# Optimization experiments

Measured on AMD Instinct MI355X. Metric: run time of the kernel, lower is better.

## Reference

```python
import jax, jax.numpy as jnp
import numpy as np

TOPK = 50
TEMP = 5.0

def _l2norm(x):
    return x / jnp.linalg.norm(x, axis=-1, keepdims=True)

def setup_inputs() -> dict:
    key = jax.random.key(0)
    k1, k2, k3 = jax.random.split(key, 3)
    b, m, d = 32, 196, 512
    n, c = 51, 1000
    return {
        "image_features": jax.random.normal(k1, (b, d), dtype=jnp.float32),
        "local_image_features": jax.random.normal(k2, (b, m, d), dtype=jnp.float32),
        "all_text_features": jax.random.normal(k3, (n, c, d), dtype=jnp.float32),
        "logit_scale": jnp.full((1,), 4.6052, dtype=jnp.float32),  # ln(100), CLIP default
    }

def reference(image_features, local_image_features, all_text_features, logit_scale):
    # Inference path of CustomCLIP.forward (labels=None) -> get_dense_logits2
    img = _l2norm(image_features)                 # [b, d]
    loc = _l2norm(local_image_features)           # [b, m, d]
    txt = _l2norm(all_text_features)              # [n, c, d]  (n = ndisc = 51)
    mean_txt = _l2norm(txt.mean(axis=0))          # [c, d]

    base_logits = img @ mean_txt.T                # [b, c]
    w_raw = jnp.einsum('bd,bmd->bm', img, loc)    # [b, m]
    txt_cnd = jnp.transpose(txt, (1, 0, 2))       # [c, n, d]
    v = jax.nn.softmax(jnp.einsum('cd,cnd->cn', mean_txt, txt_cnd) * TEMP, axis=1)  # [c, n]

    # similarity of every patch to every description, laid out with m last for top_k
    sim = jnp.einsum('bmd,cnd->bcnm', loc, txt_cnd)        # [b, c, n, m]
    sim_topk, idx_topk = jax.lax.top_k(sim, TOPK)          # [b, c, n, k] each

    b = img.shape[0]
    # gather per-image patch weights at selected patch indices: w_raw[b, idx]
    w_topk = w_raw[jnp.arange(b)[:, None, None, None], idx_topk]   # [b, c, n, k]
    w = jax.nn.softmax(w_topk * TEMP, axis=3)               # softmax over selected patches

    bias_logits = jnp.sum(sim_topk * w * v[None, :, :, None], axis=(2, 3))  # [b, c]
    return jnp.exp(logit_scale)[0] * (base_logits + bias_logits)
```

## Files before the change

kernel.cpp:

```cpp
#include <hip/hip_runtime.h>
#include <stdint.h>

typedef __bf16  bf16x8 __attribute__((ext_vector_type(8)));
typedef float   f32x4  __attribute__((ext_vector_type(4)));
typedef short   s16x2  __attribute__((ext_vector_type(2)));
typedef unsigned short u16;

#define TEMP 5.0f

__device__ inline float wsum(float v){
  #pragma unroll
  for (int off=32; off; off>>=1) v += __shfl_xor(v, off, 64);
  return v;
}
__device__ inline float wmax(float v){
  #pragma unroll
  for (int off=32; off; off>>=1) v = fmaxf(v, __shfl_xor(v, off, 64));
  return v;
}
__device__ inline u16 f2bf(float f){
  unsigned u = __float_as_uint(f);
  u = u + 0x7fffu + ((u>>16)&1u);
  return (u16)(u>>16);
}
__device__ inline float bfl(unsigned u){ return __uint_as_float(u<<16); }
__device__ inline float bfh(unsigned u){ return __uint_as_float(u & 0xffff0000u); }

__device__ inline s16x2 as_s16x2(int v){ union{int i; s16x2 v;} u; u.i=v; return u.v; }

#if __has_builtin(__builtin_amdgcn_permlane16_swap) && __has_builtin(__builtin_amdgcn_permlane32_swap)
__device__ inline int qsum_i(int c){
  auto a = __builtin_amdgcn_permlane16_swap((unsigned)c, (unsigned)c, false, false);
  c = (int)a[0] + (int)a[1];
  auto b = __builtin_amdgcn_permlane32_swap((unsigned)c, (unsigned)c, false, false);
  return (int)b[0] + (int)b[1];
}
__device__ inline float qsum_f(float v){
  auto a = __builtin_amdgcn_permlane16_swap(__float_as_uint(v), __float_as_uint(v), false, false);
  v = __uint_as_float(a[0]) + __uint_as_float(a[1]);
  auto b = __builtin_amdgcn_permlane32_swap(__float_as_uint(v), __float_as_uint(v), false, false);
  return __uint_as_float(b[0]) + __uint_as_float(b[1]);
}
__device__ inline int qmin_i(int v){
  auto a = __builtin_amdgcn_permlane16_swap((unsigned)v, (unsigned)v, false, false);
  v = min((int)a[0], (int)a[1]);
  auto b = __builtin_amdgcn_permlane32_swap((unsigned)v, (unsigned)v, false, false);
  return min((int)b[0], (int)b[1]);
}
__device__ inline int qmax_i(int v){
  auto a = __builtin_amdgcn_permlane16_swap((unsigned)v, (unsigned)v, false, false);
  v = max((int)a[0], (int)a[1]);
  auto b = __builtin_amdgcn_permlane32_swap((unsigned)v, (unsigned)v, false, false);
  return max((int)b[0], (int)b[1]);
}
#else
__device__ inline int qsum_i(int c){
  c += __shfl_xor(c, 16, 64); c += __shfl_xor(c, 32, 64); return c;
}
__device__ inline float qsum_f(float v){
  v += __shfl_xor(v, 16, 64); v += __shfl_xor(v, 32, 64); return v;
}
__device__ inline int qmin_i(int v){
  v = min(v, __shfl_xor(v, 16, 64)); v = min(v, __shfl_xor(v, 32, 64)); return v;
}
__device__ inline int qmax_i(int v){
  v = max(v, __shfl_xor(v, 16, 64)); v = max(v, __shfl_xor(v, 32, 64)); return v;
}
#endif

__device__ inline s16x2 pkmin2(s16x2 a, s16x2 b){
  s16x2 r; r.x = a.x < b.x ? a.x : b.x; r.y = a.y < b.y ? a.y : b.y; return r;
}
__device__ inline s16x2 pkmax2(s16x2 a, s16x2 b){
  s16x2 r; r.x = a.x > b.x ? a.x : b.x; r.y = a.y > b.y ? a.y : b.y; return r;
}

__device__ inline void cp16(void* lds_uniform, const void* g){
  __builtin_amdgcn_global_load_lds(
    (const __attribute__((address_space(1))) unsigned int*)g,
    (__attribute__((address_space(3))) unsigned int*)lds_uniform, 16, 0, 0);
}

__global__ void k_img(const float* __restrict__ X, float* __restrict__ imgn){
  int b = blockIdx.x, lane = threadIdx.x;
  const float* src = X + (size_t)b*512 + lane*8;
  float4 a = *(const float4*)src;
  float4 c = *(const float4*)(src+4);
  float ss = a.x*a.x+a.y*a.y+a.z*a.z+a.w*a.w + c.x*c.x+c.y*c.y+c.z*c.z+c.w*c.w;
  ss = wsum(ss);
  float inv = 1.0f/sqrtf(ss);
  float* dst = imgn + (size_t)b*512 + lane*8;
  float4 o0 = {a.x*inv,a.y*inv,a.z*inv,a.w*inv};
  float4 o1 = {c.x*inv,c.y*inv,c.z*inv,c.w*inv};
  *(float4*)dst = o0; *(float4*)(dst+4) = o1;
}

__global__ void k_txt(const float* __restrict__ X, u16* __restrict__ TXT, float* __restrict__ invn){
  int cn = blockIdx.x, lane = threadIdx.x;
  int kc = lane>>2, kk8 = (lane&3)*8;
  size_t dstE = ((size_t)kc*51008 + cn)*32 + kk8;
  if (cn >= 51000){
    uint4 z = {0,0,0,0};
    *(uint4*)(TXT + dstE) = z;
    return;
  }
  int c = cn/51, n = cn - c*51;
  const float* src = X + ((size_t)n*1000 + c)*512 + lane*8;
  float4 a = *(const float4*)src;
  float4 d = *(const float4*)(src+4);
  float ss = a.x*a.x+a.y*a.y+a.z*a.z+a.w*a.w + d.x*d.x+d.y*d.y+d.z*d.z+d.w*d.w;
  ss = wsum(ss);
  float inv = 1.0f/sqrtf(ss);
  u16 h0=f2bf(a.x*inv),h1=f2bf(a.y*inv),h2=f2bf(a.z*inv),h3=f2bf(a.w*inv);
  u16 h4=f2bf(d.x*inv),h5=f2bf(d.y*inv),h6=f2bf(d.z*inv),h7=f2bf(d.w*inv);
  uint4 o;
  o.x = (unsigned)h0 | ((unsigned)h1<<16);
  o.y = (unsigned)h2 | ((unsigned)h3<<16);
  o.z = (unsigned)h4 | ((unsigned)h5<<16);
  o.w = (unsigned)h6 | ((unsigned)h7<<16);
  *(uint4*)(TXT + dstE) = o;
  if (lane==0) invn[(size_t)n*1000 + c] = inv;
}

__global__ void k_mean(const float* __restrict__ X, const float* __restrict__ invn, float* __restrict__ MT){
  int c = blockIdx.x, tid = threadIdx.x, lane = tid&63, wv = tid>>6;
  __shared__ float sinv[51];
  __shared__ float red[4];
  if (tid < 51) sinv[tid] = invn[(size_t)tid*1000 + c];
  __syncthreads();
  int d0 = tid*2;
  float sx=0.f, sy=0.f;
  for (int n=0;n<51;++n){
    const float2 x = *(const float2*)(X + ((size_t)n*1000 + c)*512 + d0);
    float iv = sinv[n];
    sx += x.x*iv; sy += x.y*iv;
  }
  float ss = sx*sx + sy*sy;
  ss = wsum(ss);
  if (lane==0) red[wv] = ss;
  __syncthreads();
  float tot = red[0]+red[1]+red[2]+red[3];
  float inv = 1.0f/sqrtf(tot);
  float2 o = {sx*inv, sy*inv};
  *(float2*)(MT + (size_t)c*512 + d0) = o;
}

__global__ void k_v(const u16* __restrict__ TXT, const float* __restrict__ MT, float* __restrict__ vbuf){
  int c = blockIdx.x, lane = threadIdx.x;
  __shared__ float lg[51];
  const float* mp = MT + (size_t)c*512 + lane*8;
  float4 m0 = *(const float4*)mp;
  float4 m1 = *(const float4*)(mp+4);
  int kc = lane>>2, kk8 = (lane&3)*8;
  for (int n=0;n<51;++n){
    size_t e = ((size_t)kc*51008 + (size_t)(c*51+n))*32 + kk8;
    uint4 q = *(const uint4*)(TXT + e);
    float d = bfl(q.x)*m0.x + bfh(q.x)*m0.y + bfl(q.y)*m0.z + bfh(q.y)*m0.w
            + bfl(q.z)*m1.x + bfh(q.z)*m1.y + bfl(q.w)*m1.z + bfh(q.w)*m1.w;
    d = wsum(d);
    if (lane==0) lg[n] = d;
  }
  __syncthreads();
  float val = (lane<51) ? lg[lane] : -1e30f;
  float mx = wmax(val);
  float e = (lane<51) ? expf(TEMP*(val-mx)) : 0.f;
  float s = wsum(e);
  if (lane<51) vbuf[(size_t)c*51 + lane] = e/s;
}

__global__ void k_base(const float* __restrict__ imgn, const float* __restrict__ MT, float* __restrict__ bias){
  int c = blockIdx.x, lane = threadIdx.x;
  const float* mp = MT + (size_t)c*512 + lane*8;
  float4 m0 = *(const float4*)mp;
  float4 m1 = *(const float4*)(mp+4);
  for (int b=0;b<32;++b){
    const float* ip = imgn + (size_t)b*512 + lane*8;
    float4 i0 = *(const float4*)ip;
    float4 i1 = *(const float4*)(ip+4);
    float d = i0.x*m0.x+i0.y*m0.y+i0.z*m0.z+i0.w*m0.w
            + i1.x*m1.x+i1.y*m1.y+i1.z*m1.z+i1.w*m1.w;
    d = wsum(d);
    if (lane==0) bias[(size_t)b*1000 + c] = d;
  }
}

__global__ void k_loc(const float* __restrict__ L, const float* __restrict__ imgn,
                      u16* __restrict__ LOC, float* __restrict__ ewg){
  int m = blockIdx.x, b = blockIdx.y, lane = threadIdx.x;
  size_t dstE = ((size_t)(b*16 + (lane>>2))*224 + m)*32 + (lane&3)*8;
  if (m >= 196){
    uint4 z = {0,0,0,0};
    *(uint4*)(LOC + dstE) = z;
    if (lane==0) ewg[(size_t)b*224 + m] = 0.f;
    return;
  }
  const float* src = L + ((size_t)b*196 + m)*512 + lane*8;
  float4 a = *(const float4*)src;
  float4 d = *(const float4*)(src+4);
  const float* ip = imgn + (size_t)b*512 + lane*8;
  float4 i0 = *(const float4*)ip;
  float4 i1 = *(const float4*)(ip+4);
  float ss = a.x*a.x+a.y*a.y+a.z*a.z+a.w*a.w + d.x*d.x+d.y*d.y+d.z*d.z+d.w*d.w;
  float ws = a.x*i0.x+a.y*i0.y+a.z*i0.z+a.w*i0.w + d.x*i1.x+d.y*i1.y+d.z*i1.z+d.w*i1.w;
  ss = wsum(ss); ws = wsum(ws);
  float inv = 1.0f/sqrtf(ss);
  u16 h0=f2bf(a.x*inv),h1=f2bf(a.y*inv),h2=f2bf(a.z*inv),h3=f2bf(a.w*inv);
  u16 h4=f2bf(d.x*inv),h5=f2bf(d.y*inv),h6=f2bf(d.z*inv),h7=f2bf(d.w*inv);
  uint4 o;
  o.x = (unsigned)h0 | ((unsigned)h1<<16);
  o.y = (unsigned)h2 | ((unsigned)h3<<16);
  o.z = (unsigned)h4 | ((unsigned)h5<<16);
  o.w = (unsigned)h6 | ((unsigned)h7<<16);
  *(uint4*)(LOC + dstE) = o;
  if (lane==0) ewg[(size_t)b*224 + m] = expf(TEMP * ws * inv);
}

__global__ __launch_bounds__(512,8) void k_main(const u16* __restrict__ TXT, const u16* __restrict__ LOC,
                                                const float* __restrict__ ewg, const float* __restrict__ vbuf,
                                                float* __restrict__ bias){
  __shared__ __align__(16) char smem[30592];
  const int tid = threadIdx.x, lane = tid & 63, wv = tid >> 6;
  const int quad = lane >> 4, l16 = lane & 15;
  const int ms = wv >> 2, ns = wv & 3;
  const int lsw = lane ^ ((lane>>3)&3);
  const int qsw = (quad ^ ((l16>>1)&3)) * 16;

  int id = blockIdx.x, b, cnt_;
  if (id < 24576){
    int g = id >> 10, r = id & 1023;
    b = r >> 5;  cnt_ = (g << 5) + (r & 31);
  } else {
    int r = id - 24576;
    b = r / 29;  cnt_ = 768 + r % 29;
  }
  const int cn0 = cnt_ * 64;

  float* ewl = (float*)(smem + 29696);
  if (tid < 224) ewl[tid] = ewg[(size_t)b*224 + tid];

  const f32x4 zero = {0.f,0.f,0.f,0.f};
  f32x4 acc[7];
  #pragma unroll
  for (int t=0;t<7;++t) acc[t]=zero;

  const u16* Abase = LOC + (size_t)(b*16)*224*32;
  char* Albd0 = smem;
  char* Albd1 = smem + 14336;

  auto stageA = [&](int kc, char* dst){
    const char* src = (const char*)(Abase + (size_t)kc*224*32);
    #pragma unroll
    for (int j=0;j<2;++j){
      int ch0 = j*512 + wv*64;
      if (ch0 < 896)
        cp16(dst + (size_t)ch0*16, src + (size_t)(ch0 + lsw)*16);
    }
  };
  auto loadB = [&](int kc)->bf16x8{
    size_t e = ((size_t)kc*51008 + (size_t)(cn0 + 16*ns + l16))*32 + quad*8;
    return *(const bf16x8*)(TXT + e);
  };
  auto domfma = [&](const char* Ab, bf16x8 bb){
    #pragma unroll
    for (int t=0;t<7;++t){
      bf16x8 af = *(const bf16x8*)(Ab + (size_t)((112*ms + 16*t + l16)*64) + qsw);
      acc[t] = __builtin_amdgcn_mfma_f32_16x16x32_bf16(af, bb, acc[t], 0,0,0);
    }
  };

  stageA(0, Albd0);
  bf16x8 bcur = loadB(0);
  __syncthreads();

  for (int kc = 0; kc < 16; ++kc){
    char* cur = (kc & 1) ? Albd1 : Albd0;
    char* nxt = (kc & 1) ? Albd0 : Albd1;
    bf16x8 bnext;
    if (kc < 15){
      stageA(kc+1, nxt);
      bnext = loadB(kc+1);
    }
    domfma(cur, bcur);
    bcur = bnext;
    __syncthreads();
  }

  const float KSC = 15360.0f;
  int kown[7][2], koth[7][2];
  {
    unsigned* wr = (unsigned*)(void*)smem + (size_t)(((ns<<1)|(ms^1))*16*58) + l16*58 + quad*2;
    #pragma unroll
    for (int t=0;t<7;++t){
      int a0 = (int)(acc[t][0]*KSC), a1 = (int)(acc[t][1]*KSC);
      int a2 = (int)(acc[t][2]*KSC), a3 = (int)(acc[t][3]*KSC);
      uint2 o; o.x = (unsigned)((a0 & 0xffff) | (a1<<16)); o.y = (unsigned)((a2 & 0xffff) | (a3<<16));
      *(uint2*)(wr + t*8) = o;
      kown[t][0] = (int)o.x; kown[t][1] = (int)o.y;
    }
  }
  __syncthreads();
  {
    const unsigned* rd = (const unsigned*)(void*)smem + (size_t)(((ns<<1)|ms)*16*58) + l16*58 + quad*2;
    #pragma unroll
    for (int t=0;t<7;++t){
      uint2 q = *(const uint2*)(rd + t*8);
      koth[t][0] = (int)q.x;
      koth[t][1] = (int)q.y;
    }
  }

  const int PKPK = (int)0xC180C180;
  if (ms == 1){
    if (quad != 0){ kown[5][0] = PKPK; kown[5][1] = PKPK; }
    kown[6][0] = PKPK; kown[6][1] = PKPK;
  } else {
    if (quad != 0){ koth[5][0] = PKPK; koth[5][1] = PKPK; }
    koth[6][0] = PKPK; koth[6][1] = PKPK;
  }

  s16x2 vmn = as_s16x2(kown[0][0]), vmx = vmn;
  #pragma unroll
  for (int t=0;t<5;++t){
    #pragma unroll
    for (int i=0;i<2;++i){
      vmn = pkmin2(vmn, as_s16x2(kown[t][i]));  vmx = pkmax2(vmx, as_s16x2(kown[t][i]));
      vmn = pkmin2(vmn, as_s16x2(koth[t][i]));  vmx = pkmax2(vmx, as_s16x2(koth[t][i]));
    }
  }
  int kmn = min((int)vmn.x, (int)vmn.y);
  int kmx = max((int)vmx.x, (int)vmx.y);
  kmn = qmin_i(kmn); kmx = qmax_i(kmx);
  int lo = kmn - 1, hi = kmx + 1;

  float flo = 146.0f, fhi = -50.0f;
  int side = 0;
  bool done = false;

  #pragma unroll 1
  for (int it = 0; it < 14; ++it){
    float fr = flo * __builtin_amdgcn_rcpf(flo - fhi);
    fr = fminf(fmaxf(fr, 0.04f), 0.96f);
    int tm = lo + (int)(fr * (float)(hi - lo));
    tm = (tm <= lo) ? (lo + 1) : ((tm >= hi) ? (hi - 1) : tm);

    s16x2 tmv = as_s16x2((tm & 0xffff) | (tm << 16));
    s16x2 ca = {0,0};
    #pragma unroll
    for (int t=0;t<7;++t){
      ca = ca + ((as_s16x2(kown[t][0]) - tmv) >> 15);
      ca = ca + ((as_s16x2(kown[t][1]) - tmv) >> 15);
      ca = ca + ((as_s16x2(koth[t][0]) - tmv) >> 15);
      ca = ca + ((as_s16x2(koth[t][1]) - tmv) >> 15);
    }
    int clt = -((int)ca.x + (int)ca.y);
    int c = qsum_i(56 - clt);

    bool ge = (c >= 50);
    if (!done){
      if (ge){ fhi = (side==1)  ? fhi*0.5f : fhi; flo = (float)(c-50); lo = tm; side = 1; }
      else   { flo = (side==-1) ? flo*0.5f : flo; fhi = (float)(c-50); hi = tm; side = -1; }
    }
    done = done || (c == 50) || ((hi - lo) <= 1);
    if (__all(done)) break;
  }
  const int thr = lo;

  float num = 0.f, den = 0.f;
  #pragma unroll
  for (int t=0;t<7;++t){
    f32x4 eA = *(const f32x4*)(ewl + 112*ms     + 16*t + 4*quad);
    f32x4 eB = *(const f32x4*)(ewl + 112*(ms^1) + 16*t + 4*quad);
    int a0 = (kown[t][0]<<16)>>16, a1 = kown[t][0]>>16;
    int a2 = (kown[t][1]<<16)>>16, a3 = kown[t][1]>>16;
    int b0 = (koth[t][0]<<16)>>16, b1 = koth[t][0]>>16;
    int b2 = (koth[t][1]<<16)>>16, b3 = koth[t][1]>>16;
    if (a0 >= thr){ num = fmaf((float)a0, eA[0], num); den += eA[0]; }
    if (a1 >= thr){ num = fmaf((float)a1, eA[1], num); den += eA[1]; }
    if (a2 >= thr){ num = fmaf((float)a2, eA[2], num); den += eA[2]; }
    if (a3 >= thr){ num = fmaf((float)a3, eA[3], num); den += eA[3]; }
    if (b0 >= thr){ num = fmaf((float)b0, eB[0], num); den += eB[0]; }
    if (b1 >= thr){ num = fmaf((float)b1, eB[1], num); den += eB[1]; }
    if (b2 >= thr){ num = fmaf((float)b2, eB[2], num); den += eB[2]; }
    if (b3 >= thr){ num = fmaf((float)b3, eB[3], num); den += eB[3]; }
  }
  num = qsum_f(num);
  den = qsum_f(den);

  int cn = cn0 + 16*ns + l16;
  if (quad == 0 && ms == 0 && cn < 51000){
    int c = cn/51;
    atomicAdd(bias + (size_t)b*1000 + c, vbuf[cn]*(num/(den*KSC)));
  }
}

__global__ void k_out(const float* __restrict__ bias, const float* __restrict__ ls, float* __restrict__ out){
  int i = blockIdx.x*256 + threadIdx.x;
  if (i < 32000){
    float sc = expf(ls[0]);
    out[i] = sc * bias[i];
  }
}

extern "C" void kernel_launch(void* const* d_in, const int* in_sizes, int n_in,
                              void* d_out, int out_size, void* d_ws, size_t ws_size,
                              hipStream_t stream) {
  const float* img = (const float*)d_in[0];
  const float* loc = (const float*)d_in[1];
  const float* txt = (const float*)d_in[2];
  const float* ls  = (const float*)d_in[3];
  char* ws = (char*)d_ws;
  float* imgn = (float*)(ws + 0);
  float* MT   = (float*)(ws + 65536);
  float* invn = (float*)(ws + 2113536);
  float* vbuf = (float*)(ws + 2317568);
  float* ewg  = (float*)(ws + 2521600);
  float* bias = (float*)(ws + 2550272);
  u16*   TXT  = (u16*)  (ws + 2678272);
  u16*   LOC  = (u16*)  (ws + 54910464);

  k_img <<<dim3(32),      dim3(64),  0, stream>>>(img, imgn);
  k_txt <<<dim3(51008),   dim3(64),  0, stream>>>(txt, TXT, invn);
  k_mean<<<dim3(1000),    dim3(256), 0, stream>>>(txt, invn, MT);
  k_v   <<<dim3(1000),    dim3(64),  0, stream>>>(TXT, MT, vbuf);
  k_base<<<dim3(1000),    dim3(64),  0, stream>>>(imgn, MT, bias);
  k_loc <<<dim3(224,32),  dim3(64),  0, stream>>>(loc, imgn, LOC, ewg);
  k_main<<<dim3(25504),   dim3(512), 0, stream>>>(TXT, LOC, ewg, vbuf, bias);
  k_out <<<dim3(125),     dim3(256), 0, stream>>>(bias, ls, (float*)d_out);
}
```

Before: 1.063 ms.

## Split per-column top-k threshold search across 8 lanes instead of 4

Changes how the per-column top-k threshold search is spread across lanes. Each column's 224 quantized similarities were held by 4 lanes (56 values each, own plus other half). They are now spread over 8 lanes (28 values each) through a new shared-memory layout. Reductions use DPP xor-1/xor-2 moves plus one permlane16 swap in place of the two-stage permlane16/32 swap. This halves the per-lane register footprint and the packed compare work in each bisection iteration, at the cost of an extra reduction stage and a different LDS read pattern.

```diff
diff --git a/kernel.cpp b/kernel.cpp
--- a/kernel.cpp
+++ b/kernel.cpp
@@ -28,51 +28,52 @@
 
 __device__ inline s16x2 as_s16x2(int v){ union{int i; s16x2 v;} u; u.i=v; return u.v; }
 
-#if __has_builtin(__builtin_amdgcn_permlane16_swap) && __has_builtin(__builtin_amdgcn_permlane32_swap)
-__device__ inline int qsum_i(int c){
-  auto a = __builtin_amdgcn_permlane16_swap((unsigned)c, (unsigned)c, false, false);
-  c = (int)a[0] + (int)a[1];
-  auto b = __builtin_amdgcn_permlane32_swap((unsigned)c, (unsigned)c, false, false);
-  return (int)b[0] + (int)b[1];
-}
-__device__ inline float qsum_f(float v){
-  auto a = __builtin_amdgcn_permlane16_swap(__float_as_uint(v), __float_as_uint(v), false, false);
-  v = __uint_as_float(a[0]) + __uint_as_float(a[1]);
-  auto b = __builtin_amdgcn_permlane32_swap(__float_as_uint(v), __float_as_uint(v), false, false);
-  return __uint_as_float(b[0]) + __uint_as_float(b[1]);
-}
-__device__ inline int qmin_i(int v){
-  auto a = __builtin_amdgcn_permlane16_swap((unsigned)v, (unsigned)v, false, false);
-  v = min((int)a[0], (int)a[1]);
-  auto b = __builtin_amdgcn_permlane32_swap((unsigned)v, (unsigned)v, false, false);
-  return min((int)b[0], (int)b[1]);
-}
-__device__ inline int qmax_i(int v){
-  auto a = __builtin_amdgcn_permlane16_swap((unsigned)v, (unsigned)v, false, false);
-  v = max((int)a[0], (int)a[1]);
-  auto b = __builtin_amdgcn_permlane32_swap((unsigned)v, (unsigned)v, false, false);
-  return max((int)b[0], (int)b[1]);
-}
-#else
-__device__ inline int qsum_i(int c){
-  c += __shfl_xor(c, 16, 64); c += __shfl_xor(c, 32, 64); return c;
-}
-__device__ inline float qsum_f(float v){
-  v += __shfl_xor(v, 16, 64); v += __shfl_xor(v, 32, 64); return v;
-}
-__device__ inline int qmin_i(int v){
-  v = min(v, __shfl_xor(v, 16, 64)); v = min(v, __shfl_xor(v, 32, 64)); return v;
-}
-__device__ inline int qmax_i(int v){
-  v = max(v, __shfl_xor(v, 16, 64)); v = max(v, __shfl_xor(v, 32, 64)); return v;
-}
-#endif
-
 __device__ inline s16x2 pkmin2(s16x2 a, s16x2 b){
   s16x2 r; r.x = a.x < b.x ? a.x : b.x; r.y = a.y < b.y ? a.y : b.y; return r;
 }
 __device__ inline s16x2 pkmax2(s16x2 a, s16x2 b){
   s16x2 r; r.x = a.x > b.x ? a.x : b.x; r.y = a.y > b.y ? a.y : b.y; return r;
+}
+
+#if __has_builtin(__builtin_amdgcn_mov_dpp)
+__device__ inline int dxor1(int v){ return __builtin_amdgcn_mov_dpp(v, 0xB1, 0xF, 0xF, true); }
+__device__ inline int dxor2(int v){ return __builtin_amdgcn_mov_dpp(v, 0x4E, 0xF, 0xF, true); }
+#else
+__device__ inline int dxor1(int v){ return __shfl_xor(v, 1, 64); }
+__device__ inline int dxor2(int v){ return __shfl_xor(v, 2, 64); }
+#endif
+
+#if __has_builtin(__builtin_amdgcn_permlane16_swap)
+__device__ inline int x16sum_i(int c){
+  auto p = __builtin_amdgcn_permlane16_swap((unsigned)c, (unsigned)c, false, false);
+  return (int)p[0] + (int)p[1];
+}
+__device__ inline int x16min_i(int c){
+  auto p = __builtin_amdgcn_permlane16_swap((unsigned)c, (unsigned)c, false, false);
+  return min((int)p[0], (int)p[1]);
+}
+__device__ inline int x16max_i(int c){
+  auto p = __builtin_amdgcn_permlane16_swap((unsigned)c, (unsigned)c, false, false);
+  return max((int)p[0], (int)p[1]);
+}
+__device__ inline float x16sum_f(float v){
+  auto p = __builtin_amdgcn_permlane16_swap(__float_as_uint(v), __float_as_uint(v), false, false);
+  return __uint_as_float(p[0]) + __uint_as_float(p[1]);
+}
+#else
+__device__ inline int   x16sum_i(int c){ return c + __shfl_xor(c, 16, 64); }
+__device__ inline int   x16min_i(int c){ return min(c, __shfl_xor(c, 16, 64)); }
+__device__ inline int   x16max_i(int c){ return max(c, __shfl_xor(c, 16, 64)); }
+__device__ inline float x16sum_f(float v){ return v + __shfl_xor(v, 16, 64); }
+#endif
+
+__device__ inline int ssum8_i(int c){ c += dxor1(c); c += dxor2(c); return x16sum_i(c); }
+__device__ inline int smin8_i(int c){ c = min(c, dxor1(c)); c = min(c, dxor2(c)); return x16min_i(c); }
+__device__ inline int smax8_i(int c){ c = max(c, dxor1(c)); c = max(c, dxor2(c)); return x16max_i(c); }
+__device__ inline float ssum8_f(float v){
+  v += __int_as_float(dxor1(__float_as_int(v)));
+  v += __int_as_float(dxor2(__float_as_int(v)));
+  return x16sum_f(v);
 }
 
 __device__ inline void cp16(void* lds_uniform, const void* g){
@@ -221,9 +222,11 @@
   __shared__ __align__(16) char smem[30592];
   const int tid = threadIdx.x, lane = tid & 63, wv = tid >> 6;
   const int quad = lane >> 4, l16 = lane & 15;
-  const int ms = wv >> 2, ns = wv & 3;
+  const int ns = wv >> 1, ms = wv & 1;
   const int lsw = lane ^ ((lane>>3)&3);
   const int qsw = (quad ^ ((l16>>1)&3)) * 16;
+  const int sub = (lane & 3) | ((lane >> 2) & 4);
+  const int col = ((lane >> 2) & 3) | ((lane >> 3) & 4);
 
   int id = blockIdx.x, b, cnt_;
   if (id < 24576){
@@ -286,50 +289,48 @@
   }
 
   const float KSC = 15360.0f;
-  int kown[7][2], koth[7][2];
   {
-    unsigned* wr = (unsigned*)(void*)smem + (size_t)(((ns<<1)|(ms^1))*16*58) + l16*58 + quad*2;
+    unsigned* wr = (unsigned*)(void*)smem + (size_t)(ns*1856) + l16*116 + ms*56 + quad*2;
     #pragma unroll
     for (int t=0;t<7;++t){
       int a0 = (int)(acc[t][0]*KSC), a1 = (int)(acc[t][1]*KSC);
       int a2 = (int)(acc[t][2]*KSC), a3 = (int)(acc[t][3]*KSC);
       uint2 o; o.x = (unsigned)((a0 & 0xffff) | (a1<<16)); o.y = (unsigned)((a2 & 0xffff) | (a3<<16));
       *(uint2*)(wr + t*8) = o;
-      kown[t][0] = (int)o.x; kown[t][1] = (int)o.y;
     }
   }
   __syncthreads();
+
+  int kk[7][2];
   {
-    const unsigned* rd = (const unsigned*)(void*)smem + (size_t)(((ns<<1)|ms)*16*58) + l16*58 + quad*2;
-    #pragma unroll
-    for (int t=0;t<7;++t){
-      uint2 q = *(const uint2*)(rd + t*8);
-      koth[t][0] = (int)q.x;
-      koth[t][1] = (int)q.y;
-    }
-  }
-
+    const unsigned* rd = (const unsigned*)(void*)smem + (size_t)(ns*1856) + (8*ms + col)*116 + sub*14;
+    #pragma unroll
+    for (int j=0;j<7;++j){
+      uint2 q = *(const uint2*)(rd + 2*j);
+      kk[j][0] = (int)q.x;
+      kk[j][1] = (int)q.y;
+    }
+  }
   const int PKPK = (int)0xC180C180;
-  if (ms == 1){
-    if (quad != 0){ kown[5][0] = PKPK; kown[5][1] = PKPK; }
-    kown[6][0] = PKPK; kown[6][1] = PKPK;
-  } else {
-    if (quad != 0){ koth[5][0] = PKPK; koth[5][1] = PKPK; }
-    koth[6][0] = PKPK; koth[6][1] = PKPK;
-  }
-
-  s16x2 vmn = as_s16x2(kown[0][0]), vmx = vmn;
+  if (sub == 7){
+    #pragma unroll
+    for (int j=0;j<7;++j){ kk[j][0] = PKPK; kk[j][1] = PKPK; }
+  }
+
+  s16x2 vmn = as_s16x2(kk[0][0]), vmx = vmn;
   #pragma unroll
-  for (int t=0;t<5;++t){
+  for (int j=0;j<7;++j){
     #pragma unroll
     for (int i=0;i<2;++i){
-      vmn = pkmin2(vmn, as_s16x2(kown[t][i]));  vmx = pkmax2(vmx, as_s16x2(kown[t][i]));
-      vmn = pkmin2(vmn, as_s16x2(koth[t][i]));  vmx = pkmax2(vmx, as_s16x2(koth[t][i]));
+      vmn = pkmin2(vmn, as_s16x2(kk[j][i]));
+      vmx = pkmax2(vmx, as_s16x2(kk[j][i]));
     }
   }
   int kmn = min((int)vmn.x, (int)vmn.y);
   int kmx = max((int)vmx.x, (int)vmx.y);
-  kmn = qmin_i(kmn); kmx = qmax_i(kmx);
+  if (sub == 7){ kmn = 32000; kmx = -32000; }
+  kmn = smin8_i(kmn);
+  kmx = smax8_i(kmx);
   int lo = kmn - 1, hi = kmx + 1;
 
   float flo = 146.0f, fhi = -50.0f;
@@ -346,14 +347,12 @@
     s16x2 tmv = as_s16x2((tm & 0xffff) | (tm << 16));
     s16x2 ca = {0,0};
     #pragma unroll
-    for (int t=0;t<7;++t){
-      ca = ca + ((as_s16x2(kown[t][0]) - tmv) >> 15);
-      ca = ca + ((as_s16x2(kown[t][1]) - tmv) >> 15);
-      ca = ca + ((as_s16x2(koth[t][0]) - tmv) >> 15);
-      ca = ca + ((as_s16x2(koth[t][1]) - tmv) >> 15);
+    for (int j=0;j<7;++j){
+      ca = ca + ((as_s16x2(kk[j][0]) - tmv) >> 15);
+      ca = ca + ((as_s16x2(kk[j][1]) - tmv) >> 15);
     }
     int clt = -((int)ca.x + (int)ca.y);
-    int c = qsum_i(56 - clt);
+    int c = ssum8_i(28 - clt);
 
     bool ge = (c >= 50);
     if (!done){
@@ -367,27 +366,21 @@
 
   float num = 0.f, den = 0.f;
   #pragma unroll
-  for (int t=0;t<7;++t){
-    f32x4 eA = *(const f32x4*)(ewl + 112*ms     + 16*t + 4*quad);
-    f32x4 eB = *(const f32x4*)(ewl + 112*(ms^1) + 16*t + 4*quad);
-    int a0 = (kown[t][0]<<16)>>16, a1 = kown[t][0]>>16;
-    int a2 = (kown[t][1]<<16)>>16, a3 = kown[t][1]>>16;
-    int b0 = (koth[t][0]<<16)>>16, b1 = koth[t][0]>>16;
-    int b2 = (koth[t][1]<<16)>>16, b3 = koth[t][1]>>16;
-    if (a0 >= thr){ num = fmaf((float)a0, eA[0], num); den += eA[0]; }
-    if (a1 >= thr){ num = fmaf((float)a1, eA[1], num); den += eA[1]; }
-    if (a2 >= thr){ num = fmaf((float)a2, eA[2], num); den += eA[2]; }
-    if (a3 >= thr){ num = fmaf((float)a3, eA[3], num); den += eA[3]; }
-    if (b0 >= thr){ num = fmaf((float)b0, eB[0], num); den += eB[0]; }
-    if (b1 >= thr){ num = fmaf((float)b1, eB[1], num); den += eB[1]; }
-    if (b2 >= thr){ num = fmaf((float)b2, eB[2], num); den += eB[2]; }
-    if (b3 >= thr){ num = fmaf((float)b3, eB[3], num); den += eB[3]; }
-  }
-  num = qsum_f(num);
-  den = qsum_f(den);
-
-  int cn = cn0 + 16*ns + l16;
-  if (quad == 0 && ms == 0 && cn < 51000){
+  for (int j=0;j<7;++j){
+    float2 e0 = *(const float2*)(ewl + 28*sub + 4*j);
+    float2 e1 = *(const float2*)(ewl + 28*sub + 4*j + 2);
+    int a0 = (kk[j][0]<<16)>>16, a1 = kk[j][0]>>16;
+    int a2 = (kk[j][1]<<16)>>16, a3 = kk[j][1]>>16;
+    if (a0 >= thr){ num = fmaf((float)a0, e0.x, num); den += e0.x; }
+    if (a1 >= thr){ num = fmaf((float)a1, e0.y, num); den += e0.y; }
+    if (a2 >= thr){ num = fmaf((float)a2, e1.x, num); den += e1.x; }
+    if (a3 >= thr){ num = fmaf((float)a3, e1.y, num); den += e1.y; }
+  }
+  num = ssum8_f(num);
+  den = ssum8_f(den);
+
+  int cn = cn0 + 16*ns + 8*ms + col;
+  if (sub == 0 && cn < 51000){
     int c = cn/51;
     atomicAdd(bias + (size_t)b*1000 + c, vbuf[cn]*(num/(den*KSC)));
   }
```

After: 1.055 ms. Within noise of the previous version (-0.8%).
